# Kernel optimization log

Hardware: AMD Instinct MI355X
Metric: run time of the kernel (lower is better)

The kernel has to match this reference:

```python
import jax, jax.numpy as jnp
import numpy as np

HEAD_DIM = 64  # self.head_dim, used only as the attention scale
D_MODEL = 1024


def setup_inputs() -> dict:
    key = jax.random.key(0)
    ks = jax.random.split(key, 6)
    B, S_NEW, S_CACHE, D = 4, 2048, 6144, D_MODEL
    w_scale = 1.0 / np.sqrt(D)  # keep logits well-conditioned
    return {
        "hidden_states": jax.random.normal(ks[0], (B, S_NEW, D), dtype=jnp.float32),
        "cached_key": jax.random.normal(ks[1], (B, S_CACHE, D), dtype=jnp.float32),
        "cached_value": jax.random.normal(ks[2], (B, S_CACHE, D), dtype=jnp.float32),
        "Wq": jax.random.normal(ks[3], (D, D), dtype=jnp.float32) * w_scale,
        "bq": jnp.zeros((D,), dtype=jnp.float32),
        "Wk": jax.random.normal(ks[4], (D, D), dtype=jnp.float32) * w_scale,
        "bk": jnp.zeros((D,), dtype=jnp.float32),
        "Wv": jax.random.normal(ks[5], (D, D), dtype=jnp.float32) * w_scale,
        "bv": jnp.zeros((D,), dtype=jnp.float32),
    }


def reference(hidden_states, cached_key, cached_value, Wq, bq, Wk, bk, Wv, bv):
    # Cached-branch forward: project new K/V, append to cache, full attention.
    # torch.nn.Linear: x @ W.T + b
    q = jnp.einsum("bsd,ed->bse", hidden_states, Wq) + bq          # [B, Sq, D]
    new_k = jnp.einsum("bsd,ed->bse", hidden_states, Wk) + bk      # [B, Sq, D]
    new_v = jnp.einsum("bsd,ed->bse", hidden_states, Wv) + bv
    k = jnp.concatenate([cached_key, new_k], axis=1)               # [B, Skv, D]
    v = jnp.concatenate([cached_value, new_v], axis=1)
    scale = 1.0 / jnp.sqrt(jnp.asarray(HEAD_DIM, dtype=q.dtype))
    scores = jnp.einsum("bqd,bkd->bqk", q, k) * scale              # [B, Sq, Skv]
    probs = jax.nn.softmax(scores, axis=-1)
    out = jnp.einsum("bqk,bkd->bqd", probs, v)                     # [B, Sq, D]
    return out
```

## Files before the change

kernel.cpp:

```cpp
#include <hip/hip_runtime.h>
#include <stdint.h>


#define DM 1024
#define NB 4
#define SQN 2048
#define SCC 6144
#define SKV 8192
#define NSPLIT 2
#define KSP (SKV / NSPLIT)

typedef unsigned short u16;
typedef __attribute__((ext_vector_type(8))) short short8;
typedef __attribute__((ext_vector_type(4))) float f32x4;

__device__ __forceinline__ u16 f2bf(float x) {
  unsigned u = __builtin_bit_cast(unsigned, x);
  u += 0x7fffu + ((u >> 16) & 1u);
  return (u16)(u >> 16);
}

__device__ __forceinline__ ushort4 cv4(float4 v) {
  ushort4 u;
  u.x = f2bf(v.x); u.y = f2bf(v.y); u.z = f2bf(v.z); u.w = f2bf(v.w);
  return u;
}

__device__ __forceinline__ void gll16(const void* g, void* l) {
  __builtin_amdgcn_global_load_lds(
      (const __attribute__((address_space(1))) void*)g,
      (__attribute__((address_space(3))) void*)l, 16, 0, 0);
}

#define FENCE() asm volatile("" ::: "memory")
#define BARRIER()                      \
  do {                                 \
    FENCE();                           \
    __builtin_amdgcn_s_barrier();      \
    FENCE();                           \
  } while (0)

#define DSR(d, a, I) \
  asm volatile("ds_read_b128 %0, %1 offset:%2" : "=v"(d) : "v"(a), "i"(I))

#define VMC4() asm volatile("s_waitcnt vmcnt(4)" ::: "memory")
#define LGKM0()                                        \
  do {                                                 \
    asm volatile("s_waitcnt lgkmcnt(0)" ::: "memory"); \
    __builtin_amdgcn_sched_barrier(0);                 \
  } while (0)

__global__ __launch_bounds__(256) void k_prep(
    const float* __restrict__ hidden, const float* __restrict__ Wq,
    const float* __restrict__ Wk, const float* __restrict__ Wv,
    const float* __restrict__ ck, u16* __restrict__ Hb,
    u16* __restrict__ Wall, u16* __restrict__ Kb, float* __restrict__ sums) {
  const long NH = (long)NB * SQN * DM / 4;
  const long NW = (long)DM * DM / 4;
  const long NC = (long)NB * SCC * DM / 4;
  const long T1 = NH + 3 * NW;
  const long T2 = T1 + NC;
  const long T3 = T2 + (long)NB * SQN / 4;
  long i = (long)blockIdx.x * 256 + threadIdx.x;
  const long st = (long)gridDim.x * 256;
  for (; i < T3; i += st) {
    if (i < NH) {
      ((ushort4*)Hb)[i] = cv4(((const float4*)hidden)[i]);
    } else if (i < T1) {
      long r = i - NH;
      int w = (int)(r / NW);
      long o = r - (long)w * NW;
      const float* src = w == 0 ? Wq : (w == 1 ? Wk : Wv);
      ((ushort4*)Wall)[r] = cv4(((const float4*)src)[o]);
    } else if (i < T2) {
      long r = i - T1;
      float4 v = ((const float4*)ck)[r];
      long e = r * 4;
      int b = (int)(e / ((long)SCC * DM));
      long rem = e - (long)b * SCC * DM;
      *(ushort4*)(Kb + (long)b * SKV * DM + rem) = cv4(v);
    } else {
      float4 z;
      z.x = 0.f; z.y = 0.f; z.z = 0.f; z.w = 0.f;
      ((float4*)sums)[i - T2] = z;
    }
  }
}

__global__ __launch_bounds__(256) void k_build_vt(const float* __restrict__ cv,
                                                  u16* __restrict__ VT) {
  __shared__ u16 t[64][65];
  const int kv0 = blockIdx.x * 64;
  const int d0 = blockIdx.y * 64;
  const int b = blockIdx.z;
  const int c = threadIdx.x & 63;
  const int r4 = threadIdx.x >> 6;
#pragma unroll
  for (int p = 0; p < 16; ++p) {
    int kr = p * 4 + r4;
    t[kr][c] = f2bf(cv[((long)b * SCC + kv0 + kr) * DM + d0 + c]);
  }
  __syncthreads();
#pragma unroll
  for (int p = 0; p < 16; ++p) {
    int dr = p * 4 + r4;
    VT[((long)b * DM + d0 + dr) * SKV + kv0 + c] = t[c][dr];
  }
}

template <int MODE>
__global__ __launch_bounds__(512, 2) void k_gemm8(
    const u16* __restrict__ A, const u16* __restrict__ B0,
    void* __restrict__ C0, void* __restrict__ C1, void* __restrict__ C2,
    float* __restrict__ sums, const float* __restrict__ bias0,
    const float* __restrict__ bias1, const float* __restrict__ bias2) {
  extern __shared__ char smem[];
  const int tid = threadIdx.x;
  const int lane = tid & 63;
  const int wv = tid >> 6;
  const int wr = wv >> 2;
  const int wc = wv & 3;
  const int bm = (MODE == 1 ? blockIdx.x : blockIdx.y) * 256;
  const int bn = (MODE == 1 ? blockIdx.y : blockIdx.x) * 256;
  const int z = blockIdx.z;

  constexpr int LD = (MODE == 2) ? SKV : DM;
  constexpr int NT = ((MODE == 2) ? KSP : DM) / 64;

  const u16 *Ab_, *Bb_;
  if constexpr (MODE == 0) {
    Ab_ = A + (long)bm * LD;
    Bb_ = B0 + (long)bn * LD;
  } else if constexpr (MODE == 1) {
    Ab_ = A + ((long)z * SKV + bm) * LD;
    Bb_ = B0 + ((long)z * SQN + bn) * LD;
  } else {
    const int bb_ = z / NSPLIT, sp = z % NSPLIT;
    Ab_ = A + ((long)bb_ * SQN + bm) * (long)SKV + (long)sp * KSP;
    Bb_ = B0 + ((long)bb_ * DM + bn) * (long)SKV + (long)sp * KSP;
  }

  const int sg = tid >> 3;
  const int ssl = ((tid & 7) ^ (sg & 7)) * 8;
  const u16* gA[2][2];
  const u16* gB[2][2];
#pragma unroll
  for (int mh = 0; mh < 2; ++mh)
#pragma unroll
    for (int g = 0; g < 2; ++g) {
      gA[mh][g] = Ab_ + (long)(g * 128 + mh * 64 + sg) * LD + ssl;
      gB[mh][g] = Bb_ + (long)((g * 2 + (sg >> 5)) * 64 + mh * 32 + (sg & 31)) * LD + ssl;
    }
  u16* lA = (u16*)smem + tid * 8;
  u16* lB = (u16*)smem + 32768 + tid * 8;

#define SA(MH, BUFN, KO)                                              \
  do {                                                                \
    gll16(gA[MH][0] + (KO), lA + (BUFN)*16384 + (MH)*8192);           \
    gll16(gA[MH][1] + (KO), lA + (BUFN)*16384 + (MH)*8192 + 4096);    \
  } while (0)
#define SB(NH, BUFN, KO)                                              \
  do {                                                                \
    gll16(gB[NH][0] + (KO), lB + (BUFN)*16384 + (NH)*8192);           \
    gll16(gB[NH][1] + (KO), lB + (BUFN)*16384 + (NH)*8192 + 4096);    \
  } while (0)

  SA(0, 0, 0);
  SB(0, 0, 0);
  SB(1, 0, 0);
  SA(1, 0, 0);
  VMC4();
  BARRIER();

  f32x4 acc[8][4];
#pragma unroll
  for (int m = 0; m < 8; ++m)
#pragma unroll
    for (int n = 0; n < 4; ++n)
#pragma unroll
      for (int j = 0; j < 4; ++j) acc[m][n][j] = 0.0f;

  const int alane = lane & 15;
  const int sw = lane & 7;
  const int s0 = lane >> 4;
  const int slot0 = ((s0 ^ sw) * 16);
  const int slot1 = (((s0 + 4) ^ sw) * 16);
  const int aBase = (wr * 64 + alane) * 128;
  const int bBase = (wc * 32 + alane) * 128;

  short8 aF[4][2];
  short8 bF[2][2][2];

#define ARD8(MH, AR0, AR1)                           \
  _Pragma("unroll") for (int ms = 0; ms < 4; ++ms) { \
    DSR(aF[ms][0], AR0, (MH)*16384 + ms * 2048);     \
    DSR(aF[ms][1], AR1, (MH)*16384 + ms * 2048);     \
  }
#define BRD4(NH, BR0, BR1)                           \
  _Pragma("unroll") for (int ns = 0; ns < 2; ++ns) { \
    DSR(bF[NH][ns][0], BR0, (NH)*16384 + ns * 2048); \
    DSR(bF[NH][ns][1], BR1, (NH)*16384 + ns * 2048); \
  }
#define MFMA_Q(MH, NH)                                                     \
  do {                                                                     \
    __builtin_amdgcn_s_setprio(1);                                         \
    _Pragma("unroll") for (int ms = 0; ms < 4; ++ms)                       \
    _Pragma("unroll") for (int ns = 0; ns < 2; ++ns)                       \
    _Pragma("unroll") for (int kk = 0; kk < 2; ++kk)                       \
        acc[(MH)*4 + ms][(NH)*2 + ns] =                                    \
            __builtin_amdgcn_mfma_f32_16x16x32_bf16(                       \
                aF[ms][kk], bF[NH][ns][kk], acc[(MH)*4 + ms][(NH)*2 + ns], \
                0, 0, 0);                                                  \
    __builtin_amdgcn_s_setprio(0);                                         \
    __builtin_amdgcn_sched_barrier(0);                                     \
  } while (0)

#define TILE_BODY(BUF, KT)                                            \
  do {                                                                \
    const long ko = (long)(((KT) + 1 < NT) ? (KT) + 1 : (KT)) * 64;   \
    const int aR0 = (BUF)*32768 + aBase + slot0;                      \
    const int aR1 = (BUF)*32768 + aBase + slot1;                      \
    const int bR0 = 65536 + (BUF)*32768 + bBase + slot0;              \
    const int bR1 = 65536 + (BUF)*32768 + bBase + slot1;              \
                                                  \
    ARD8(0, aR0, aR1);                                                \
    BRD4(0, bR0, bR1);                                                \
    SA(0, (BUF) ^ 1, ko);                                             \
    VMC4();                                                           \
    BARRIER();                                                        \
    LGKM0();                                                          \
    MFMA_Q(0, 0);                                                     \
                                                  \
    BRD4(1, bR0, bR1);                                                \
    SB(0, (BUF) ^ 1, ko);                                             \
    VMC4();                                                           \
    BARRIER();                                                        \
    LGKM0();                                                          \
    MFMA_Q(0, 1);                                                     \
                                                  \
    ARD8(1, aR0, aR1);                                                \
    SB(1, (BUF) ^ 1, ko);                                             \
    BARRIER();                                                        \
    LGKM0();                                                          \
    MFMA_Q(1, 1);                                                     \
                                 \
    SA(1, (BUF) ^ 1, ko);                                             \
    VMC4();                                                           \
    BARRIER();                                                        \
    MFMA_Q(1, 0);                                                     \
  } while (0)

  for (int t2 = 0; t2 < NT; t2 += 2) {
    TILE_BODY(0, t2);
    TILE_BODY(1, t2 + 1);
  }
#undef TILE_BODY
#undef ARD8
#undef BRD4
#undef MFMA_Q
#undef SA
#undef SB

  const int rsub = (lane >> 4) * 4;

  if constexpr (MODE == 0) {
    const int which = bm >> 10;
    const float* bp = which == 0 ? bias0 : (which == 1 ? bias1 : bias2);
    u16* Cq = (u16*)C0;
    u16* Ck = (u16*)C1;
    u16* Cvt = (u16*)C2;
    const int od_base = (bm & 1023) + wr * 128 + rsub;
    if (which == 2) {
#pragma unroll
      for (int n = 0; n < 4; ++n) {
        int token = bn + wc * 64 + n * 16 + alane;
        int b = token >> 11, ss = token & 2047;
        u16* vtb = Cvt + (long)b * DM * SKV + SCC + ss;
#pragma unroll
        for (int m = 0; m < 8; ++m) {
          int cc = od_base + m * 16;
          float4 bb = *(const float4*)(bp + cc);
          float bv4[4] = {bb.x, bb.y, bb.z, bb.w};
#pragma unroll
          for (int jj = 0; jj < 4; ++jj)
            vtb[(long)(cc + jj) * SKV] = f2bf(acc[m][n][jj] + bv4[jj]);
        }
      }
    } else {
#pragma unroll
      for (int n = 0; n < 4; ++n) {
        int token = bn + wc * 64 + n * 16 + alane;
        u16* dst;
        if (which == 1) {
          int b = token >> 11, ss = token & 2047;
          dst = Ck + ((long)b * SKV + SCC + ss) * DM;
        } else {
          dst = Cq + (long)token * DM;
        }
#pragma unroll
        for (int m = 0; m < 8; ++m) {
          int cc = od_base + m * 16;
          float4 bb = *(const float4*)(bp + cc);
          ushort4 u;
          u.x = f2bf(acc[m][n][0] + bb.x);
          u.y = f2bf(acc[m][n][1] + bb.y);
          u.z = f2bf(acc[m][n][2] + bb.z);
          u.w = f2bf(acc[m][n][3] + bb.w);
          *(ushort4*)(dst + cc) = u;
        }
      }
    }
  } else if constexpr (MODE == 1) {
    u16* Pp = (u16*)C0 + (long)z * SQN * SKV;
    float* sb = sums + z * SQN;
    const float CE = 0.18033688011112042f;
    const int kv_base = bm + wr * 128 + rsub;
#pragma unroll
    for (int n = 0; n < 4; ++n) {
      int q = bn + wc * 64 + n * 16 + alane;
      u16* prow = Pp + (long)q * SKV;
      float part = 0.f;
#pragma unroll
      for (int m = 0; m < 8; ++m) {
        int kv = kv_base + m * 16;
        float e0 = exp2f(acc[m][n][0] * CE);
        float e1 = exp2f(acc[m][n][1] * CE);
        float e2 = exp2f(acc[m][n][2] * CE);
        float e3 = exp2f(acc[m][n][3] * CE);
        part += (e0 + e1) + (e2 + e3);
        ushort4 u;
        u.x = f2bf(e0); u.y = f2bf(e1); u.z = f2bf(e2); u.w = f2bf(e3);
        *(ushort4*)(prow + kv) = u;
      }
      part += __shfl_xor(part, 16);
      part += __shfl_xor(part, 32);
      if ((lane >> 4) == 0) atomicAdd(&sb[q], part);
    }
  } else {
    float* Cp = (float*)C0 + (long)z * SQN * DM;
#pragma unroll
    for (int n = 0; n < 4; ++n) {
      int col = bn + wc * 64 + n * 16 + alane;
#pragma unroll
      for (int m = 0; m < 8; ++m)
#pragma unroll
        for (int j = 0; j < 4; ++j) {
          int row = bm + wr * 128 + m * 16 + rsub + j;
          Cp[(long)row * DM + col] = acc[m][n][j];
        }
    }
  }
}

__global__ __launch_bounds__(256) void k_reduce(const float* __restrict__ Op,
                                                const float* __restrict__ sums,
                                                float* __restrict__ out) {
  const long n4 = (long)NB * SQN * DM / 4;
  long i = (long)blockIdx.x * 256 + threadIdx.x;
  if (i >= n4) return;
  long e = i * 4;
  int b = (int)(e / ((long)SQN * DM));
  long rem = e - (long)b * SQN * DM;
  int row = (int)(rem / DM);
  const long z4 = (long)SQN * DM / 4;
  long i0 = (long)(b * NSPLIT) * z4 + (rem >> 2);
  float4 a0 = ((const float4*)Op)[i0];
  float4 a1 = ((const float4*)Op)[i0 + z4];
  float inv = 1.0f / sums[b * SQN + row];
  float4 r;
  r.x = (a0.x + a1.x) * inv;
  r.y = (a0.y + a1.y) * inv;
  r.z = (a0.z + a1.z) * inv;
  r.w = (a0.w + a1.w) * inv;
  ((float4*)out)[i] = r;
}

extern "C" void kernel_launch(void* const* d_in, const int* in_sizes, int n_in,
                              void* d_out, int out_size, void* d_ws, size_t ws_size,
                              hipStream_t stream) {
  const float* hidden = (const float*)d_in[0];
  const float* ck = (const float*)d_in[1];
  const float* cv = (const float*)d_in[2];
  const float* Wq = (const float*)d_in[3];
  const float* bq = (const float*)d_in[4];
  const float* Wk = (const float*)d_in[5];
  const float* bk = (const float*)d_in[6];
  const float* Wv = (const float*)d_in[7];
  const float* bv = (const float*)d_in[8];
  (void)in_sizes; (void)n_in; (void)out_size; (void)ws_size;

  hipFuncSetAttribute(reinterpret_cast<const void*>(&k_gemm8<0>),
                      hipFuncAttributeMaxDynamicSharedMemorySize, 131072);
  hipFuncSetAttribute(reinterpret_cast<const void*>(&k_gemm8<1>),
                      hipFuncAttributeMaxDynamicSharedMemorySize, 131072);
  hipFuncSetAttribute(reinterpret_cast<const void*>(&k_gemm8<2>),
                      hipFuncAttributeMaxDynamicSharedMemorySize, 131072);

  char* base = (char*)d_ws;
  size_t off = 0;
  auto alloc = [&](size_t bytes) {
    char* p = base + off;
    off = (off + bytes + 255) & ~(size_t)255;
    return p;
  };
  u16* Hb = (u16*)alloc((size_t)NB * SQN * DM * 2);
  u16* Wall = (u16*)alloc((size_t)3 * DM * DM * 2);
  u16* Qb = (u16*)alloc((size_t)NB * SQN * DM * 2);
  u16* Kb = (u16*)alloc((size_t)NB * SKV * DM * 2);
  float* Opart = (float*)base;
  size_t opart_bytes = (size_t)NB * NSPLIT * SQN * DM * 4;
  if (off < opart_bytes) off = (opart_bytes + 255) & ~(size_t)255;
  u16* VT = (u16*)alloc((size_t)NB * DM * SKV * 2);
  u16* P = (u16*)alloc((size_t)NB * SQN * SKV * 2);
  float* sums = (float*)alloc((size_t)NB * SQN * 4);

  k_prep<<<2048, 256, 0, stream>>>(hidden, Wq, Wk, Wv, ck, Hb, Wall, Kb, sums);

  k_gemm8<0><<<dim3(32, 12, 1), 512, 131072, stream>>>(
      Wall, Hb, Qb, Kb, VT, nullptr, bq, bk, bv);

  k_build_vt<<<dim3(SCC / 64, DM / 64, NB), 256, 0, stream>>>(cv, VT);

  k_gemm8<1><<<dim3(SKV / 256, SQN / 256, NB), 512, 131072, stream>>>(
      Kb, Qb, P, nullptr, nullptr, sums, nullptr, nullptr, nullptr);

  k_gemm8<2><<<dim3(DM / 256, SQN / 256, NB * NSPLIT), 512, 131072, stream>>>(
      P, VT, Opart, nullptr, nullptr, nullptr, nullptr, nullptr, nullptr);

  k_reduce<<<(NB * SQN * DM / 4 + 255) / 256, 256, 0, stream>>>(
      Opart, sums, (float*)d_out);
}
```

Before: 403.3 us.

## Replace split-K PV GEMM and reduce kernel with a 256x128-tile full-K kernel

The P·V stage is now a dedicated kernel using 256x128 output tiles over the full 8192-long K dimension, replacing the 256x256 split-K GEMM plus a separate reduction kernel. The 1/sum normalisation is fused into the epilogue, so the fp32 partial outputs are no longer written and re-read. The grid size stays the same (256 blocks), but each block runs twice as many K iterations with smaller tiles and less LDS. That lowers arithmetic intensity per block and adds B traffic in exchange for dropping the partial-sum memory traffic and one launch.

Measured after the change: 429.9 us. 6.6% more time.

```diff
diff --git a/kernel.cpp b/kernel.cpp
--- a/kernel.cpp
+++ b/kernel.cpp
@@ -7,8 +7,6 @@
 #define SQN 2048
 #define SCC 6144
 #define SKV 8192
-#define NSPLIT 2
-#define KSP (SKV / NSPLIT)
 
 typedef unsigned short u16;
 typedef __attribute__((ext_vector_type(8))) short short8;
@@ -43,7 +41,7 @@
 #define DSR(d, a, I) \
   asm volatile("ds_read_b128 %0, %1 offset:%2" : "=v"(d) : "v"(a), "i"(I))
 
-#define VMC4() asm volatile("s_waitcnt vmcnt(4)" ::: "memory")
+#define VMCN(N) asm volatile("s_waitcnt vmcnt(" #N ")" ::: "memory")
 #define LGKM0()                                        \
   do {                                                 \
     asm volatile("s_waitcnt lgkmcnt(0)" ::: "memory"); \
@@ -124,20 +122,16 @@
   const int bn = (MODE == 1 ? blockIdx.y : blockIdx.x) * 256;
   const int z = blockIdx.z;
 
-  constexpr int LD = (MODE == 2) ? SKV : DM;
-  constexpr int NT = ((MODE == 2) ? KSP : DM) / 64;
+  constexpr int LD = DM;
+  constexpr int NT = DM / 64;
 
   const u16 *Ab_, *Bb_;
   if constexpr (MODE == 0) {
     Ab_ = A + (long)bm * LD;
     Bb_ = B0 + (long)bn * LD;
-  } else if constexpr (MODE == 1) {
+  } else {
     Ab_ = A + ((long)z * SKV + bm) * LD;
     Bb_ = B0 + ((long)z * SQN + bn) * LD;
-  } else {
-    const int bb_ = z / NSPLIT, sp = z % NSPLIT;
-    Ab_ = A + ((long)bb_ * SQN + bm) * (long)SKV + (long)sp * KSP;
-    Bb_ = B0 + ((long)bb_ * DM + bn) * (long)SKV + (long)sp * KSP;
   }
 
   const int sg = tid >> 3;
@@ -169,7 +163,7 @@
   SB(0, 0, 0);
   SB(1, 0, 0);
   SA(1, 0, 0);
-  VMC4();
+  VMCN(4);
   BARRIER();
 
   f32x4 acc[8][4];
@@ -222,30 +216,26 @@
     const int aR1 = (BUF)*32768 + aBase + slot1;                      \
     const int bR0 = 65536 + (BUF)*32768 + bBase + slot0;              \
     const int bR1 = 65536 + (BUF)*32768 + bBase + slot1;              \
-                                                  \
     ARD8(0, aR0, aR1);                                                \
     BRD4(0, bR0, bR1);                                                \
     SA(0, (BUF) ^ 1, ko);                                             \
-    VMC4();                                                           \
+    VMCN(4);                                                          \
     BARRIER();                                                        \
     LGKM0();                                                          \
     MFMA_Q(0, 0);                                                     \
-                                                  \
     BRD4(1, bR0, bR1);                                                \
     SB(0, (BUF) ^ 1, ko);                                             \
-    VMC4();                                                           \
+    VMCN(4);                                                          \
     BARRIER();                                                        \
     LGKM0();                                                          \
     MFMA_Q(0, 1);                                                     \
-                                                  \
     ARD8(1, aR0, aR1);                                                \
     SB(1, (BUF) ^ 1, ko);                                             \
     BARRIER();                                                        \
     LGKM0();                                                          \
     MFMA_Q(1, 1);                                                     \
-                                 \
     SA(1, (BUF) ^ 1, ko);                                             \
-    VMC4();                                                           \
+    VMCN(4);                                                          \
     BARRIER();                                                        \
     MFMA_Q(1, 0);                                                     \
   } while (0)
@@ -310,7 +300,7 @@
         }
       }
     }
-  } else if constexpr (MODE == 1) {
+  } else {
     u16* Pp = (u16*)C0 + (long)z * SQN * SKV;
     float* sb = sums + z * SQN;
     const float CE = 0.18033688011112042f;
@@ -336,43 +326,161 @@
       part += __shfl_xor(part, 32);
       if ((lane >> 4) == 0) atomicAdd(&sb[q], part);
     }
-  } else {
-    float* Cp = (float*)C0 + (long)z * SQN * DM;
-#pragma unroll
-    for (int n = 0; n < 4; ++n) {
-      int col = bn + wc * 64 + n * 16 + alane;
-#pragma unroll
-      for (int m = 0; m < 8; ++m)
-#pragma unroll
-        for (int j = 0; j < 4; ++j) {
-          int row = bm + wr * 128 + m * 16 + rsub + j;
-          Cp[(long)row * DM + col] = acc[m][n][j];
-        }
+  }
+}
+
+__global__ __launch_bounds__(512, 2) void k_pv(
+    const u16* __restrict__ P, const u16* __restrict__ VT,
+    const float* __restrict__ sums, float* __restrict__ out) {
+  extern __shared__ char smem[];
+  const int tid = threadIdx.x;
+  const int lane = tid & 63;
+  const int wv = tid >> 6;
+  const int wr = wv >> 1;
+  const int wc = wv & 1;
+  const int bm = blockIdx.y * 256;
+  const int bn = blockIdx.x * 128;
+  const int z = blockIdx.z;
+  constexpr int NT = SKV / 64;
+
+  const u16* Ab_ = P + ((long)z * SQN + bm) * (long)SKV;
+  const u16* Bb_ = VT + ((long)z * DM + bn) * (long)SKV;
+
+  const int sg = tid >> 3;
+  const int ssl = ((tid & 7) ^ (sg & 7)) * 8;
+  const u16* gA[2][2];
+  const u16* gB[2];
+#pragma unroll
+  for (int mh = 0; mh < 2; ++mh)
+#pragma unroll
+    for (int g = 0; g < 2; ++g)
+      gA[mh][g] = Ab_ + (long)((g * 2 + (sg >> 5)) * 64 + mh * 32 + (sg & 31)) * SKV + ssl;
+#pragma unroll
+  for (int nh = 0; nh < 2; ++nh)
+    gB[nh] = Bb_ + (long)((sg >> 5) * 64 + nh * 32 + (sg & 31)) * SKV + ssl;
+
+  u16* lA = (u16*)smem + tid * 8;
+  u16* lB = (u16*)smem + 32768 + tid * 8;
+
+#define SAP(MH, BUFN, KO)                                             \
+  do {                                                                \
+    gll16(gA[MH][0] + (KO), lA + (BUFN)*16384 + (MH)*8192);           \
+    gll16(gA[MH][1] + (KO), lA + (BUFN)*16384 + (MH)*8192 + 4096);    \
+  } while (0)
+#define SBP(NH, BUFN, KO) \
+  gll16(gB[NH] + (KO), lB + (BUFN)*8192 + (NH)*4096)
+
+  SAP(0, 0, 0);
+  SBP(0, 0, 0);
+  SBP(1, 0, 0);
+  SAP(1, 0, 0);
+  VMCN(3);
+  BARRIER();
+
+  f32x4 acc[4][4];
+#pragma unroll
+  for (int m = 0; m < 4; ++m)
+#pragma unroll
+    for (int n = 0; n < 4; ++n)
+#pragma unroll
+      for (int j = 0; j < 4; ++j) acc[m][n][j] = 0.0f;
+
+  const int alane = lane & 15;
+  const int sw = lane & 7;
+  const int s0 = lane >> 4;
+  const int slot0 = ((s0 ^ sw) * 16);
+  const int slot1 = (((s0 + 4) ^ sw) * 16);
+  const int aBase = (wr * 32 + alane) * 128;
+  const int bBase = (wc * 32 + alane) * 128;
+
+  short8 aF[2][2];
+  short8 bF[2][2][2];
+
+#define ARD4(MH, AR0, AR1)                           \
+  _Pragma("unroll") for (int ml = 0; ml < 2; ++ml) { \
+    DSR(aF[ml][0], AR0, (MH)*16384 + ml * 2048);     \
+    DSR(aF[ml][1], AR1, (MH)*16384 + ml * 2048);     \
+  }
+#define BRD4P(NH, BR0, BR1)                          \
+  _Pragma("unroll") for (int nl = 0; nl < 2; ++nl) { \
+    DSR(bF[NH][nl][0], BR0, (NH)*8192 + nl * 2048);  \
+    DSR(bF[NH][nl][1], BR1, (NH)*8192 + nl * 2048);  \
+  }
+#define MFMA_Q8(MH, NH)                                                    \
+  do {                                                                     \
+    __builtin_amdgcn_s_setprio(1);                                         \
+    _Pragma("unroll") for (int ml = 0; ml < 2; ++ml)                       \
+    _Pragma("unroll") for (int nl = 0; nl < 2; ++nl)                       \
+    _Pragma("unroll") for (int kk = 0; kk < 2; ++kk)                       \
+        acc[(MH)*2 + ml][(NH)*2 + nl] =                                    \
+            __builtin_amdgcn_mfma_f32_16x16x32_bf16(                       \
+                aF[ml][kk], bF[NH][nl][kk], acc[(MH)*2 + ml][(NH)*2 + nl], \
+                0, 0, 0);                                                  \
+    __builtin_amdgcn_s_setprio(0);                                         \
+    __builtin_amdgcn_sched_barrier(0);                                     \
+  } while (0)
+
+#define TILE_PV(BUF, KT)                                              \
+  do {                                                                \
+    const long ko = (long)(((KT) + 1 < NT) ? (KT) + 1 : (KT)) * 64;   \
+    const int aR0 = (BUF)*32768 + aBase + slot0;                      \
+    const int aR1 = (BUF)*32768 + aBase + slot1;                      \
+    const int bR0 = 65536 + (BUF)*16384 + bBase + slot0;              \
+    const int bR1 = 65536 + (BUF)*16384 + bBase + slot1;              \
+                                                  \
+    ARD4(0, aR0, aR1);                                                \
+    BRD4P(0, bR0, bR1);                                               \
+    SAP(0, (BUF) ^ 1, ko);                                            \
+    VMCN(4);                                                          \
+    BARRIER();                                                        \
+    LGKM0();                                                          \
+    MFMA_Q8(0, 0);                                                    \
+                                                  \
+    BRD4P(1, bR0, bR1);                                               \
+    SBP(0, (BUF) ^ 1, ko);                                            \
+    VMCN(3);                                                          \
+    BARRIER();                                                        \
+    LGKM0();                                                          \
+    MFMA_Q8(0, 1);                                                    \
+                                                  \
+    ARD4(1, aR0, aR1);                                                \
+    SBP(1, (BUF) ^ 1, ko);                                            \
+    BARRIER();                                                        \
+    LGKM0();                                                          \
+    MFMA_Q8(1, 1);                                                    \
+                                                  \
+    SAP(1, (BUF) ^ 1, ko);                                            \
+    VMCN(3);                                                          \
+    BARRIER();                                                        \
+    MFMA_Q8(1, 0);                                                    \
+  } while (0)
+
+  for (int t2 = 0; t2 < NT; t2 += 2) {
+    TILE_PV(0, t2);
+    TILE_PV(1, t2 + 1);
+  }
+#undef TILE_PV
+#undef ARD4
+#undef BRD4P
+#undef MFMA_Q8
+#undef SAP
+#undef SBP
+
+  const int rsub = (lane >> 4) * 4;
+  float* Cp = out + (long)z * SQN * DM;
+  const float* sb = sums + z * SQN;
+#pragma unroll
+  for (int m = 0; m < 4; ++m)
+#pragma unroll
+    for (int j = 0; j < 4; ++j) {
+      int row = bm + wr * 64 + m * 16 + rsub + j;
+      float inv = 1.0f / sb[row];
+#pragma unroll
+      for (int n = 0; n < 4; ++n) {
+        int col = bn + wc * 64 + n * 16 + alane;
+        Cp[(long)row * DM + col] = acc[m][n][j] * inv;
+      }
     }
-  }
-}
-
-__global__ __launch_bounds__(256) void k_reduce(const float* __restrict__ Op,
-                                                const float* __restrict__ sums,
-                                                float* __restrict__ out) {
-  const long n4 = (long)NB * SQN * DM / 4;
-  long i = (long)blockIdx.x * 256 + threadIdx.x;
-  if (i >= n4) return;
-  long e = i * 4;
-  int b = (int)(e / ((long)SQN * DM));
-  long rem = e - (long)b * SQN * DM;
-  int row = (int)(rem / DM);
-  const long z4 = (long)SQN * DM / 4;
-  long i0 = (long)(b * NSPLIT) * z4 + (rem >> 2);
-  float4 a0 = ((const float4*)Op)[i0];
-  float4 a1 = ((const float4*)Op)[i0 + z4];
-  float inv = 1.0f / sums[b * SQN + row];
-  float4 r;
-  r.x = (a0.x + a1.x) * inv;
-  r.y = (a0.y + a1.y) * inv;
-  r.z = (a0.z + a1.z) * inv;
-  r.w = (a0.w + a1.w) * inv;
-  ((float4*)out)[i] = r;
 }
 
 extern "C" void kernel_launch(void* const* d_in, const int* in_sizes, int n_in,
@@ -393,8 +501,8 @@
                       hipFuncAttributeMaxDynamicSharedMemorySize, 131072);
   hipFuncSetAttribute(reinterpret_cast<const void*>(&k_gemm8<1>),
                       hipFuncAttributeMaxDynamicSharedMemorySize, 131072);
-  hipFuncSetAttribute(reinterpret_cast<const void*>(&k_gemm8<2>),
-                      hipFuncAttributeMaxDynamicSharedMemorySize, 131072);
+  hipFuncSetAttribute(reinterpret_cast<const void*>(&k_pv),
+                      hipFuncAttributeMaxDynamicSharedMemorySize, 98304);
 
   char* base = (char*)d_ws;
   size_t off = 0;
@@ -407,9 +515,6 @@
   u16* Wall = (u16*)alloc((size_t)3 * DM * DM * 2);
   u16* Qb = (u16*)alloc((size_t)NB * SQN * DM * 2);
   u16* Kb = (u16*)alloc((size_t)NB * SKV * DM * 2);
-  float* Opart = (float*)base;
-  size_t opart_bytes = (size_t)NB * NSPLIT * SQN * DM * 4;
-  if (off < opart_bytes) off = (opart_bytes + 255) & ~(size_t)255;
   u16* VT = (u16*)alloc((size_t)NB * DM * SKV * 2);
   u16* P = (u16*)alloc((size_t)NB * SQN * SKV * 2);
   float* sums = (float*)alloc((size_t)NB * SQN * 4);
@@ -424,9 +529,6 @@
   k_gemm8<1><<<dim3(SKV / 256, SQN / 256, NB), 512, 131072, stream>>>(
       Kb, Qb, P, nullptr, nullptr, sums, nullptr, nullptr, nullptr);
 
-  k_gemm8<2><<<dim3(DM / 256, SQN / 256, NB * NSPLIT), 512, 131072, stream>>>(
-      P, VT, Opart, nullptr, nullptr, nullptr, nullptr, nullptr, nullptr);
-
-  k_reduce<<<(NB * SQN * DM / 4 + 255) / 256, 256, 0, stream>>>(
-      Opart, sums, (float*)d_out);
-}
+  k_pv<<<dim3(DM / 128, SQN / 256, NB), 512, 98304, stream>>>(
+      P, VT, sums, (float*)d_out);
+}
```
